# Kernel tuning notes

Measured on AMD Instinct MI355X. Metric: run time of the kernel, lower is better.

Reference implementation:

```python
import jax, jax.numpy as jnp
import numpy as np

N_NODES = 50000
N_EDGES = 800000
D_IN = 128
D_OUT = 128


def setup_inputs() -> dict:
    key = jax.random.key(0)
    k_x, k_r, k_c, k_v, k_w = jax.random.split(key, 5)
    x = jax.random.normal(k_x, (N_NODES, D_IN), dtype=jnp.float32)
    edge_row = jax.random.randint(k_r, (N_EDGES,), 0, N_NODES)  # destination nodes
    edge_col = jax.random.randint(k_c, (N_EDGES,), 0, N_NODES)  # source nodes
    edge_val = jax.random.uniform(k_v, (N_EDGES,), dtype=jnp.float32)
    W = jax.random.normal(k_w, (D_OUT, D_IN), dtype=jnp.float32) * (1.0 / np.sqrt(D_IN))
    bias = jnp.zeros((D_OUT,), dtype=jnp.float32)
    return {"x": x, "edge_row": edge_row, "edge_col": edge_col,
            "edge_val": edge_val, "W": W, "bias": bias}


def reference(x, edge_row, edge_col, edge_val, W, bias):
    # support = linear(x)   (nn.Linear with bias=False: x @ W.T)
    support = jnp.einsum('ni,oi->no', x, W)  # [N, D_OUT]
    # out = sparse.mm(adj, support): gather source rows, scale by edge value,
    # scatter-add into destination rows.
    msgs = edge_val[:, None] * support[edge_col]  # [E, D_OUT]
    out = jax.ops.segment_sum(msgs, edge_row, num_segments=N_NODES)
    return out + bias
```

## Files before the change

kernel.cpp:

```cpp
#include <hip/hip_runtime.h>
#include <hip/hip_bf16.h>


constexpr int D     = 128;
constexpr int NPB   = 64;
constexpr int CAP   = 2048;
constexpr int C1    = 3200;
constexpr int BT    = 1024;
constexpr int NBMAX = 1024;

__device__ inline unsigned int bf1(float f) {
    unsigned int u = __float_as_uint(f);
    return (u + 0x7fffu + ((u >> 16) & 1u)) >> 16;
}
__device__ inline unsigned int bf2(float lo, float hi) {
    return bf1(lo) | (bf1(hi) << 16);
}
__device__ inline unsigned int cvt2(float a, float b) {
    __hip_bfloat162 h = __float22bfloat162_rn(float2{a, b});
    return *reinterpret_cast<unsigned int*>(&h);
}
__device__ inline float bflo(unsigned int u) { return __uint_as_float(u << 16); }
__device__ inline float bfhi(unsigned int u) { return __uint_as_float(u & 0xffff0000u); }

__global__ __launch_bounds__(256) void cvt_bf16_kernel(const float* __restrict__ in,
                                                       uint4* __restrict__ out, int n8,
                                                       int* __restrict__ gcursor, int nb) {
    int i = blockIdx.x * 256 + threadIdx.x;
    if (i < nb) gcursor[i] = 0;
    if (i >= n8) return;
    const float4* p = (const float4*)in + (size_t)i * 2;
    float4 a = p[0], b = p[1];
    uint4 r;
    r.x = cvt2(a.x, a.y); r.y = cvt2(a.z, a.w);
    r.z = cvt2(b.x, b.y); r.w = cvt2(b.z, b.w);
    out[i] = r;
}

__global__ __launch_bounds__(256) void gemm_mfma_kernel(const float* __restrict__ x,
                                                        const unsigned short* __restrict__ Wb,
                                                        unsigned short* __restrict__ supb,
                                                        int n_nodes) {
    using frag  = __attribute__((ext_vector_type(8))) short;
    using f32x4 = __attribute__((ext_vector_type(4))) float;
    union FU { uint4 u; frag f; };
    const int wv = threadIdx.x >> 6;
    const int lane = threadIdx.x & 63;
    const int m = lane & 15, quad = lane >> 4;
    const int row0 = blockIdx.x * 128 + wv * 32;
    const int r0 = min(row0 + m, n_nodes - 1);
    const int r1 = min(row0 + 16 + m, n_nodes - 1);

    frag a0[4], a1[4];
#pragma unroll
    for (int kf = 0; kf < 4; ++kf) {
        const float4* xp0 = (const float4*)(x + (size_t)r0 * D + kf * 32 + quad * 8);
        float4 p = xp0[0], q = xp0[1];
        FU t;
        t.u.x = cvt2(p.x, p.y); t.u.y = cvt2(p.z, p.w);
        t.u.z = cvt2(q.x, q.y); t.u.w = cvt2(q.z, q.w);
        a0[kf] = t.f;
        const float4* xp1 = (const float4*)(x + (size_t)r1 * D + kf * 32 + quad * 8);
        p = xp1[0]; q = xp1[1];
        t.u.x = cvt2(p.x, p.y); t.u.y = cvt2(p.z, p.w);
        t.u.z = cvt2(q.x, q.y); t.u.w = cvt2(q.z, q.w);
        a1[kf] = t.f;
    }

    f32x4 acc0[8], acc1[8];
#pragma unroll
    for (int ct = 0; ct < 8; ++ct) {
        acc0[ct] = (f32x4){0.f, 0.f, 0.f, 0.f};
        acc1[ct] = (f32x4){0.f, 0.f, 0.f, 0.f};
    }

#pragma unroll
    for (int ct = 0; ct < 8; ++ct) {
        const unsigned short* wrow = Wb + (size_t)(ct * 16 + m) * D;
#pragma unroll
        for (int kf = 0; kf < 4; ++kf) {
            frag b = *(const frag*)(wrow + kf * 32 + quad * 8);
            acc0[ct] = __builtin_amdgcn_mfma_f32_16x16x32_bf16(a0[kf], b, acc0[ct], 0, 0, 0);
            acc1[ct] = __builtin_amdgcn_mfma_f32_16x16x32_bf16(a1[kf], b, acc1[ct], 0, 0, 0);
        }
    }

#pragma unroll
    for (int ct = 0; ct < 8; ++ct) {
#pragma unroll
        for (int r = 0; r < 4; ++r) {
            int rr0 = row0 + quad * 4 + r;
            if (rr0 < n_nodes)
                supb[(size_t)rr0 * D + ct * 16 + m] = (unsigned short)bf1(acc0[ct][r]);
            int rr1 = row0 + 16 + quad * 4 + r;
            if (rr1 < n_nodes)
                supb[(size_t)rr1 * D + ct * 16 + m] = (unsigned short)bf1(acc1[ct][r]);
        }
    }
}

__global__ __launch_bounds__(BT) void binpass_kernel(const int* __restrict__ erow,
                                                     const int* __restrict__ ecol,
                                                     const float* __restrict__ eval,
                                                     int* __restrict__ gcursor,
                                                     int2* __restrict__ coarse,
                                                     int n_edges, int nb) {
    __shared__ int bkcnt[NBMAX];
    __shared__ int bkoff[NBMAX];
    __shared__ int wsum[16];
    __shared__ int gbase[NBMAX];
    __shared__ unsigned short slotbk[C1];
    __shared__ int2 stage[C1];
    const int t = threadIdx.x;
    const int base = blockIdx.x * C1;
    const int m = min(C1, n_edges - base);

    for (int i = t; i < nb; i += BT) bkcnt[i] = 0;
    __syncthreads();

    constexpr int EPT = (C1 + BT - 1) / BT;
    int  bk[EPT], rank[EPT];
    int2 pk[EPT];
#pragma unroll
    for (int j = 0; j < EPT; ++j) {
        int i = t + j * BT;
        bk[j] = -1;
        if (i < m) {
            int e = base + i;
            int dst = erow[e];
            int b = dst / NPB;
            bk[j] = b;
            rank[j] = atomicAdd(&bkcnt[b], 1);
            pk[j] = make_int2(ecol[e] | ((dst & (NPB - 1)) << 20),
                              __float_as_int(eval[e]));
        }
    }
    __syncthreads();

    {
        const int w = t >> 6, l = t & 63;
        int v = (t < nb) ? bkcnt[t] : 0;
        int inc = v;
#pragma unroll
        for (int o = 1; o < 64; o <<= 1) {
            int u = __shfl_up(inc, o, 64);
            if (l >= o) inc += u;
        }
        if (l == 63) wsum[w] = inc;
        __syncthreads();
        if (t < 16) {
            int wv2 = wsum[t];
            int winc = wv2;
#pragma unroll
            for (int o = 1; o < 16; o <<= 1) {
                int u = __shfl_up(winc, o, 16);
                if (t >= o) winc += u;
            }
            wsum[t] = winc - wv2;
        }
        __syncthreads();
        if (t < nb) bkoff[t] = inc - v + wsum[w];
    }
    __syncthreads();

#pragma unroll
    for (int j = 0; j < EPT; ++j) {
        if (bk[j] >= 0) {
            int s = bkoff[bk[j]] + rank[j];
            stage[s] = pk[j];
            slotbk[s] = (unsigned short)bk[j];
        }
    }
    if (t < nb) {
        int c = bkcnt[t];
        gbase[t] = (c > 0) ? (t * CAP + atomicAdd(&gcursor[t], c)) : 0;
    }
    __syncthreads();

    for (int i = t; i < m; i += BT) {
        int b = slotbk[i];
        int p = gbase[b] + (i - bkoff[b]);
        if (p < (b + 1) * CAP) coarse[p] = stage[i];
    }
}

__global__ __launch_bounds__(BT) void sortgather_kernel(const int* __restrict__ gcursor,
                                                        const int2* __restrict__ coarse,
                                                        const unsigned short* __restrict__ supb,
                                                        const float* __restrict__ bias,
                                                        float* __restrict__ out,
                                                        int n_nodes) {
    __shared__ int ncnt[NPB];
    __shared__ int noff[NPB];
    __shared__ int ncur[NPB];
    __shared__ int2 sorted[CAP];
    const int t = threadIdx.x;
    const int b = blockIdx.x;
    const int node0 = b * NPB;
    const int m = min(gcursor[b], CAP);
    const int2* src = coarse + (size_t)b * CAP;

    if (t < NPB) ncnt[t] = 0;
    __syncthreads();

    for (int i = t; i < m; i += BT)
        atomicAdd(&ncnt[(src[i].x >> 20) & (NPB - 1)], 1);
    __syncthreads();

    if (t < NPB) {
        int v = ncnt[t];
        int inc = v;
        for (int o = 1; o < NPB; o <<= 1) {
            int u = __shfl_up(inc, o, 64);
            if (t >= o) inc += u;
        }
        noff[t] = inc - v;
        ncur[t] = inc - v;
    }
    __syncthreads();

    for (int i = t; i < m; i += BT) {
        int2 e = src[i];
        int dl = (e.x >> 20) & (NPB - 1);
        int p = atomicAdd(&ncur[dl], 1);
        sorted[p] = make_int2(e.x & 0xFFFFF, e.y);
    }
    __syncthreads();

    const int qw = t >> 4;
    const int l16 = t & 15;
    const int node = node0 + qw;
    if (node >= n_nodes) return;
    const int beg = noff[qw];
    const int end = beg + ncnt[qw];

    const float4* b4 = (const float4*)(bias + l16 * 8);
    float4 acc0 = b4[0], acc1 = b4[1];

    int e = beg;
    for (; e + 1 < end; e += 2) {
        int2 d0 = sorted[e], d1 = sorted[e + 1];
        uint4 u0 = *(const uint4*)(supb + (size_t)d0.x * D + l16 * 8);
        uint4 u1 = *(const uint4*)(supb + (size_t)d1.x * D + l16 * 8);
        float v0 = __int_as_float(d0.y), v1 = __int_as_float(d1.y);
        acc0.x += v0 * bflo(u0.x) + v1 * bflo(u1.x);
        acc0.y += v0 * bfhi(u0.x) + v1 * bfhi(u1.x);
        acc0.z += v0 * bflo(u0.y) + v1 * bflo(u1.y);
        acc0.w += v0 * bfhi(u0.y) + v1 * bfhi(u1.y);
        acc1.x += v0 * bflo(u0.z) + v1 * bflo(u1.z);
        acc1.y += v0 * bfhi(u0.z) + v1 * bfhi(u1.z);
        acc1.z += v0 * bflo(u0.w) + v1 * bflo(u1.w);
        acc1.w += v0 * bfhi(u0.w) + v1 * bfhi(u1.w);
    }
    if (e < end) {
        int2 d0 = sorted[e];
        uint4 u0 = *(const uint4*)(supb + (size_t)d0.x * D + l16 * 8);
        float v0 = __int_as_float(d0.y);
        acc0.x += v0 * bflo(u0.x); acc0.y += v0 * bfhi(u0.x);
        acc0.z += v0 * bflo(u0.y); acc0.w += v0 * bfhi(u0.y);
        acc1.x += v0 * bflo(u0.z); acc1.y += v0 * bfhi(u0.z);
        acc1.z += v0 * bflo(u0.w); acc1.w += v0 * bfhi(u0.w);
    }
    float4* o4 = (float4*)(out + (size_t)node * D + l16 * 8);
    o4[0] = acc0;
    o4[1] = acc1;
}

__global__ __launch_bounds__(256) void init_out_kernel(float4* __restrict__ out4,
                                                       const float4* __restrict__ bias4,
                                                       int total4) {
    int i = blockIdx.x * 256 + threadIdx.x;
    if (i < total4) out4[i] = bias4[i & 31];
}

__global__ __launch_bounds__(256) void scatter_fb_kernel(const int* __restrict__ erow,
                                                         const int* __restrict__ ecol,
                                                         const float* __restrict__ eval,
                                                         const unsigned short* __restrict__ supb,
                                                         float* __restrict__ out,
                                                         int n_edges) {
    int e = blockIdx.x * 8 + (threadIdx.x >> 5);
    if (e >= n_edges) return;
    int lane = threadIdx.x & 31;
    int src = ecol[e], dst = erow[e];
    float v = eval[e];
    const unsigned short* sp = supb + (size_t)src * D + lane * 4;
    float* op = out + (size_t)dst * D + lane * 4;
#pragma unroll
    for (int j = 0; j < 4; ++j)
        atomicAdd(op + j, v * __uint_as_float(((unsigned)sp[j]) << 16));
}

static inline size_t align_up(size_t v, size_t a) { return (v + a - 1) & ~(a - 1); }

extern "C" void kernel_launch(void* const* d_in, const int* in_sizes, int n_in,
                              void* d_out, int out_size, void* d_ws, size_t ws_size,
                              hipStream_t stream) {
    const float* x    = (const float*)d_in[0];
    const int*   erow = (const int*)d_in[1];
    const int*   ecol = (const int*)d_in[2];
    const float* eval = (const float*)d_in[3];
    const float* W    = (const float*)d_in[4];
    const float* bias = (const float*)d_in[5];
    float* out = (float*)d_out;

    const int n_nodes = in_sizes[0] / D;
    const int n_edges = in_sizes[1];
    const int nb = (n_nodes + NPB - 1) / NPB;

    char* base = (char*)d_ws;
    size_t off = 0;
    unsigned short* supb = (unsigned short*)(base + off); off = align_up(off + (size_t)n_nodes * D * 2, 256);
    unsigned short* Wb   = (unsigned short*)(base + off); off = align_up(off + (size_t)D * D * 2, 256);
    int*  gcursor = (int*)(base + off);  off = align_up(off + (size_t)nb * 4, 256);
    int2* coarse  = (int2*)(base + off); off = align_up(off + (size_t)nb * CAP * 8, 256);

    const int n8 = D * D / 8;
    const int cvt_grid = (max(n8, nb) + 255) / 256;
    const bool fast = (n_nodes < (1 << 20)) && (nb <= NBMAX) && (off <= ws_size);

    cvt_bf16_kernel<<<cvt_grid, 256, 0, stream>>>(W, (uint4*)Wb, n8, gcursor, fast ? nb : 0);
    gemm_mfma_kernel<<<(n_nodes + 127) / 128, 256, 0, stream>>>(x, Wb, supb, n_nodes);

    if (fast) {
        binpass_kernel<<<(n_edges + C1 - 1) / C1, BT, 0, stream>>>(
            erow, ecol, eval, gcursor, coarse, n_edges, nb);
        sortgather_kernel<<<nb, BT, 0, stream>>>(
            gcursor, coarse, supb, bias, out, n_nodes);
    } else {
        int total4 = n_nodes * (D / 4);
        init_out_kernel<<<(total4 + 255) / 256, 256, 0, stream>>>(
            (float4*)out, (const float4*)bias, total4);
        scatter_fb_kernel<<<(n_edges + 7) / 8, 256, 0, stream>>>(
            erow, ecol, eval, supb, out, n_edges);
    }
}
```

Measured before the change: 142.3 us.

## Fuse W bf16 conversion and cursor reset into GEMM, register-cache edges in sort

Removes the separate conversion kernel. The GEMM now reads fp32 W and converts it to bf16 inline, and block 0 zeroes the bin cursors. Full tiles skip the row-bound clamps and store checks. In the sort-gather kernel, each thread keeps its edges in registers between the counting pass and the scatter pass, so the coarse bin is not read from global memory twice. The cost is redundant W conversion in every GEMM block, twice the W load bytes, and more register use.

```diff
diff --git a/kernel.cpp b/kernel.cpp
--- a/kernel.cpp
+++ b/kernel.cpp
@@ -13,9 +13,6 @@
     unsigned int u = __float_as_uint(f);
     return (u + 0x7fffu + ((u >> 16) & 1u)) >> 16;
 }
-__device__ inline unsigned int bf2(float lo, float hi) {
-    return bf1(lo) | (bf1(hi) << 16);
-}
 __device__ inline unsigned int cvt2(float a, float b) {
     __hip_bfloat162 h = __float22bfloat162_rn(float2{a, b});
     return *reinterpret_cast<unsigned int*>(&h);
@@ -23,33 +20,26 @@
 __device__ inline float bflo(unsigned int u) { return __uint_as_float(u << 16); }
 __device__ inline float bfhi(unsigned int u) { return __uint_as_float(u & 0xffff0000u); }
 
-__global__ __launch_bounds__(256) void cvt_bf16_kernel(const float* __restrict__ in,
-                                                       uint4* __restrict__ out, int n8,
-                                                       int* __restrict__ gcursor, int nb) {
-    int i = blockIdx.x * 256 + threadIdx.x;
-    if (i < nb) gcursor[i] = 0;
-    if (i >= n8) return;
-    const float4* p = (const float4*)in + (size_t)i * 2;
-    float4 a = p[0], b = p[1];
-    uint4 r;
-    r.x = cvt2(a.x, a.y); r.y = cvt2(a.z, a.w);
-    r.z = cvt2(b.x, b.y); r.w = cvt2(b.z, b.w);
-    out[i] = r;
-}
-
 __global__ __launch_bounds__(256) void gemm_mfma_kernel(const float* __restrict__ x,
-                                                        const unsigned short* __restrict__ Wb,
+                                                        const float* __restrict__ W,
                                                         unsigned short* __restrict__ supb,
-                                                        int n_nodes) {
+                                                        int n_nodes,
+                                                        int* __restrict__ gcursor, int nb) {
     using frag  = __attribute__((ext_vector_type(8))) short;
     using f32x4 = __attribute__((ext_vector_type(4))) float;
     union FU { uint4 u; frag f; };
+
+    if (blockIdx.x == 0) {
+        for (int i = threadIdx.x; i < nb; i += 256) gcursor[i] = 0;
+    }
+
     const int wv = threadIdx.x >> 6;
     const int lane = threadIdx.x & 63;
     const int m = lane & 15, quad = lane >> 4;
     const int row0 = blockIdx.x * 128 + wv * 32;
-    const int r0 = min(row0 + m, n_nodes - 1);
-    const int r1 = min(row0 + 16 + m, n_nodes - 1);
+    const bool full = (row0 + 32 <= n_nodes);
+    const int r0 = full ? row0 + m      : min(row0 + m, n_nodes - 1);
+    const int r1 = full ? row0 + 16 + m : min(row0 + 16 + m, n_nodes - 1);
 
     frag a0[4], a1[4];
 #pragma unroll
@@ -76,25 +66,41 @@
 
 #pragma unroll
     for (int ct = 0; ct < 8; ++ct) {
-        const unsigned short* wrow = Wb + (size_t)(ct * 16 + m) * D;
+        const float* wrow = W + (size_t)(ct * 16 + m) * D;
 #pragma unroll
         for (int kf = 0; kf < 4; ++kf) {
-            frag b = *(const frag*)(wrow + kf * 32 + quad * 8);
-            acc0[ct] = __builtin_amdgcn_mfma_f32_16x16x32_bf16(a0[kf], b, acc0[ct], 0, 0, 0);
-            acc1[ct] = __builtin_amdgcn_mfma_f32_16x16x32_bf16(a1[kf], b, acc1[ct], 0, 0, 0);
-        }
-    }
-
-#pragma unroll
-    for (int ct = 0; ct < 8; ++ct) {
-#pragma unroll
-        for (int r = 0; r < 4; ++r) {
-            int rr0 = row0 + quad * 4 + r;
-            if (rr0 < n_nodes)
+            const float4* wp = (const float4*)(wrow + kf * 32 + quad * 8);
+            float4 p = wp[0], q = wp[1];
+            FU t;
+            t.u.x = cvt2(p.x, p.y); t.u.y = cvt2(p.z, p.w);
+            t.u.z = cvt2(q.x, q.y); t.u.w = cvt2(q.z, q.w);
+            acc0[ct] = __builtin_amdgcn_mfma_f32_16x16x32_bf16(a0[kf], t.f, acc0[ct], 0, 0, 0);
+            acc1[ct] = __builtin_amdgcn_mfma_f32_16x16x32_bf16(a1[kf], t.f, acc1[ct], 0, 0, 0);
+        }
+    }
+
+    if (full) {
+#pragma unroll
+        for (int ct = 0; ct < 8; ++ct) {
+#pragma unroll
+            for (int r = 0; r < 4; ++r) {
+                int rr0 = row0 + quad * 4 + r;
                 supb[(size_t)rr0 * D + ct * 16 + m] = (unsigned short)bf1(acc0[ct][r]);
-            int rr1 = row0 + 16 + quad * 4 + r;
-            if (rr1 < n_nodes)
-                supb[(size_t)rr1 * D + ct * 16 + m] = (unsigned short)bf1(acc1[ct][r]);
+                supb[(size_t)(rr0 + 16) * D + ct * 16 + m] = (unsigned short)bf1(acc1[ct][r]);
+            }
+        }
+    } else {
+#pragma unroll
+        for (int ct = 0; ct < 8; ++ct) {
+#pragma unroll
+            for (int r = 0; r < 4; ++r) {
+                int rr0 = row0 + quad * 4 + r;
+                if (rr0 < n_nodes)
+                    supb[(size_t)rr0 * D + ct * 16 + m] = (unsigned short)bf1(acc0[ct][r]);
+                int rr1 = rr0 + 16;
+                if (rr1 < n_nodes)
+                    supb[(size_t)rr1 * D + ct * 16 + m] = (unsigned short)bf1(acc1[ct][r]);
+            }
         }
     }
 }
@@ -203,8 +209,19 @@
     if (t < NPB) ncnt[t] = 0;
     __syncthreads();
 
-    for (int i = t; i < m; i += BT)
-        atomicAdd(&ncnt[(src[i].x >> 20) & (NPB - 1)], 1);
+    constexpr int EPT2 = CAP / BT;
+    int2 ee[EPT2];
+    int  dl[EPT2];
+#pragma unroll
+    for (int j = 0; j < EPT2; ++j) {
+        int i = t + j * BT;
+        dl[j] = -1;
+        if (i < m) {
+            ee[j] = src[i];
+            dl[j] = (ee[j].x >> 20) & (NPB - 1);
+            atomicAdd(&ncnt[dl[j]], 1);
+        }
+    }
     __syncthreads();
 
     if (t < NPB) {
@@ -219,11 +236,12 @@
     }
     __syncthreads();
 
-    for (int i = t; i < m; i += BT) {
-        int2 e = src[i];
-        int dl = (e.x >> 20) & (NPB - 1);
-        int p = atomicAdd(&ncur[dl], 1);
-        sorted[p] = make_int2(e.x & 0xFFFFF, e.y);
+#pragma unroll
+    for (int j = 0; j < EPT2; ++j) {
+        if (dl[j] >= 0) {
+            int p = atomicAdd(&ncur[dl[j]], 1);
+            sorted[p] = make_int2(ee[j].x & 0xFFFFF, ee[j].y);
+        }
     }
     __syncthreads();
 
@@ -311,16 +329,13 @@
     char* base = (char*)d_ws;
     size_t off = 0;
     unsigned short* supb = (unsigned short*)(base + off); off = align_up(off + (size_t)n_nodes * D * 2, 256);
-    unsigned short* Wb   = (unsigned short*)(base + off); off = align_up(off + (size_t)D * D * 2, 256);
     int*  gcursor = (int*)(base + off);  off = align_up(off + (size_t)nb * 4, 256);
     int2* coarse  = (int2*)(base + off); off = align_up(off + (size_t)nb * CAP * 8, 256);
 
-    const int n8 = D * D / 8;
-    const int cvt_grid = (max(n8, nb) + 255) / 256;
     const bool fast = (n_nodes < (1 << 20)) && (nb <= NBMAX) && (off <= ws_size);
 
-    cvt_bf16_kernel<<<cvt_grid, 256, 0, stream>>>(W, (uint4*)Wb, n8, gcursor, fast ? nb : 0);
-    gemm_mfma_kernel<<<(n_nodes + 127) / 128, 256, 0, stream>>>(x, Wb, supb, n_nodes);
+    gemm_mfma_kernel<<<(n_nodes + 127) / 128, 256, 0, stream>>>(
+        x, W, supb, n_nodes, gcursor, fast ? nb : 0);
 
     if (fast) {
         binpass_kernel<<<(n_edges + C1 - 1) / C1, BT, 0, stream>>>(
```

Measured after the change: 147.6 us. +3.7%, slower.
